# Performance work log

Measured on AMD Instinct MI355X. Metric: run time of the kernel, lower is better.

Reference implementation:

```python
import jax, jax.numpy as jnp
import numpy as np

OBS_DIM = 512
ATTN_DIM = 128


def setup_inputs() -> dict:
    key = jax.random.key(0)
    k1, k2, k3, k4 = jax.random.split(key, 4)
    agent_observation = jax.random.normal(k1, (128, 32, 512), dtype=jnp.float32)
    visible_observations = jax.random.normal(k2, (128, 32, 16, 512), dtype=jnp.float32)
    # learned bilinear projection params (match torch.randn init)
    w_psi = jax.random.normal(k3, (OBS_DIM, ATTN_DIM), dtype=jnp.float32)
    w_phi = jax.random.normal(k4, (OBS_DIM, ATTN_DIM), dtype=jnp.float32)
    return {
        "agent_observation": agent_observation,
        "visible_observations": visible_observations,
        "w_psi": w_psi,
        "w_phi": w_phi,
    }


def reference(agent_observation, visible_observations, w_psi, w_phi):
    # beta[b,e,a] = agent_obs[b,e] @ W_psi @ W_phi^T @ visible[b,e,a]
    q = jnp.einsum("bed,dk->bek", agent_observation, w_psi)          # (B,E,K)
    kv = jnp.einsum("bead,dk->beak", visible_observations, w_phi)    # (B,E,A,K)
    betas = jnp.einsum("bek,beak->bea", q, kv)                       # (B,E,A)
    # softmax over the visible-agent axis (the inner loop axis, dim=1 of
    # the per-entity stacked beta matrix in the original code)
    return jax.nn.softmax(betas, axis=-1)
```

## Files before the change

### kernel.cpp

```cpp
#include <hip/hip_runtime.h>
#include <math.h>

#define OBS 512
#define ATT 128
#define RPB 4

__global__ void transpose_wphi_k(const float* __restrict__ wphi,
                                 float* __restrict__ wphiT) {
  int idx = blockIdx.x * 256 + threadIdx.x;
  int k  = idx >> 9;
  int dd = idx & 511;
  wphiT[idx] = wphi[dd * ATT + k];
}

__device__ __forceinline__ void fma4(float4& a, float s, float4 w) {
  a.x = fmaf(s, w.x, a.x);
  a.y = fmaf(s, w.y, a.y);
  a.z = fmaf(s, w.z, a.z);
  a.w = fmaf(s, w.w, a.w);
}

__launch_bounds__(256, 4)
__global__ void entity_attn_k(const float* __restrict__ A,
                              const float* __restrict__ V,
                              const float* __restrict__ Wpsi,
                              const float* __restrict__ WphiT,
                              float* __restrict__ Out)
{
  __shared__ __align__(16) float S[6656];

  const int tid  = threadIdx.x;
  const int lane = tid & 63;
  const int wave = tid >> 6;
  const int g0   = blockIdx.x * RPB;

  {
    const int r = tid & 3;
    const int c = tid >> 2;
    const float4* a4 = (const float4*)(A + (size_t)(g0 + r) * OBS) + c * 2;
    float4 v0 = a4[0], v1 = a4[1];
    const int d0 = c * 8;
    S[(d0+0)*4+r] = v0.x; S[(d0+1)*4+r] = v0.y;
    S[(d0+2)*4+r] = v0.z; S[(d0+3)*4+r] = v0.w;
    S[(d0+4)*4+r] = v1.x; S[(d0+5)*4+r] = v1.y;
    S[(d0+6)*4+r] = v1.z; S[(d0+7)*4+r] = v1.w;
  }
  __syncthreads();

  {
    const int kg = tid & 31;
    const int ds = tid >> 5;
    float4 acc0 = make_float4(0.f,0.f,0.f,0.f);
    float4 acc1 = acc0, acc2 = acc0, acc3 = acc0;
    const float4* wp4 = (const float4*)Wpsi;
    const float4* at4 = (const float4*)S;
    const int dbase = ds * 64;
#pragma unroll 8
    for (int i = 0; i < 64; ++i) {
      const int d = dbase + i;
      float4 w = wp4[d * 32 + kg];
      float4 a = at4[d];
      fma4(acc0, a.x, w);
      fma4(acc1, a.y, w);
      fma4(acc2, a.z, w);
      fma4(acc3, a.w, w);
    }
    float4* qp4 = (float4*)(S + 2048);
    qp4[(ds*4+0)*32 + kg] = acc0;
    qp4[(ds*4+1)*32 + kg] = acc1;
    qp4[(ds*4+2)*32 + kg] = acc2;
    qp4[(ds*4+3)*32 + kg] = acc3;
  }
  __syncthreads();

  {
#pragma unroll
    for (int e = tid; e < 512; e += 256) {
      const int r = e & 3;
      const int k = e >> 2;
      float s = 0.f;
#pragma unroll
      for (int ds = 0; ds < 8; ++ds) s += S[2048 + (ds*4 + r)*128 + k];
      S[6144 + k*4 + r] = s;
    }
  }
  __syncthreads();

  {
    float acc[8] = {0.f,0.f,0.f,0.f,0.f,0.f,0.f,0.f};
    const float4* qt4 = (const float4*)(S + 6144);
#pragma unroll 4
    for (int k = 0; k < 128; ++k) {
      float w0 = WphiT[k*512 + tid];
      float w1 = WphiT[k*512 + tid + 256];
      float4 q = qt4[k];
      acc[0] = fmaf(q.x, w0, acc[0]);
      acc[1] = fmaf(q.y, w0, acc[1]);
      acc[2] = fmaf(q.z, w0, acc[2]);
      acc[3] = fmaf(q.w, w0, acc[3]);
      acc[4] = fmaf(q.x, w1, acc[4]);
      acc[5] = fmaf(q.y, w1, acc[5]);
      acc[6] = fmaf(q.z, w1, acc[6]);
      acc[7] = fmaf(q.w, w1, acc[7]);
    }
#pragma unroll
    for (int r = 0; r < 4; ++r) {
      S[r*512 + tid]       = acc[r];
      S[r*512 + tid + 256] = acc[4+r];
    }
  }
  __syncthreads();

  {
    const int r = wave;
    const size_t g = (size_t)(g0 + r);
    const float4* vrow = (const float4*)V + g * 2048;
    const float4* ur   = (const float4*)S + r * 128;
    const float4 uf0 = ur[lane*2];
    const float4 uf1 = ur[lane*2 + 1];
    float acc[16];
#pragma unroll
    for (int ag = 0; ag < 4; ++ag) {
      float4 va[8];
#pragma unroll
      for (int j = 0; j < 4; ++j) {
        va[j*2]   = vrow[(ag*4 + j)*128 + lane*2];
        va[j*2+1] = vrow[(ag*4 + j)*128 + lane*2 + 1];
      }
#pragma unroll
      for (int j = 0; j < 4; ++j) {
        float s;
        s = uf0.x * va[j*2].x;
        s = fmaf(uf0.y, va[j*2].y, s);
        s = fmaf(uf0.z, va[j*2].z, s);
        s = fmaf(uf0.w, va[j*2].w, s);
        s = fmaf(uf1.x, va[j*2+1].x, s);
        s = fmaf(uf1.y, va[j*2+1].y, s);
        s = fmaf(uf1.z, va[j*2+1].z, s);
        s = fmaf(uf1.w, va[j*2+1].w, s);
        acc[ag*4 + j] = s;
      }
    }
#pragma unroll
    for (int a = 0; a < 16; ++a) {
      float v = acc[a];
      v += __shfl_xor(v, 32, 64);
      v += __shfl_xor(v, 16, 64);
      v += __shfl_xor(v,  8, 64);
      v += __shfl_xor(v,  4, 64);
      v += __shfl_xor(v,  2, 64);
      v += __shfl_xor(v,  1, 64);
      acc[a] = v;
    }
    float mx = acc[0];
#pragma unroll
    for (int a = 1; a < 16; ++a) mx = fmaxf(mx, acc[a]);
    float ssum = 0.f;
#pragma unroll
    for (int a = 0; a < 16; ++a) { acc[a] = __expf(acc[a] - mx); ssum += acc[a]; }
    const float inv = 1.0f / ssum;
    if (lane == 0) {
      float4* o4 = (float4*)(Out + g * 16);
      o4[0] = make_float4(acc[0]*inv,  acc[1]*inv,  acc[2]*inv,  acc[3]*inv);
      o4[1] = make_float4(acc[4]*inv,  acc[5]*inv,  acc[6]*inv,  acc[7]*inv);
      o4[2] = make_float4(acc[8]*inv,  acc[9]*inv,  acc[10]*inv, acc[11]*inv);
      o4[3] = make_float4(acc[12]*inv, acc[13]*inv, acc[14]*inv, acc[15]*inv);
    }
  }
}

extern "C" void kernel_launch(void* const* d_in, const int* in_sizes, int n_in,
                              void* d_out, int out_size, void* d_ws, size_t ws_size,
                              hipStream_t stream) {
  (void)in_sizes; (void)n_in; (void)out_size; (void)ws_size;
  const float* A    = (const float*)d_in[0];
  const float* V    = (const float*)d_in[1];
  const float* Wpsi = (const float*)d_in[2];
  const float* Wphi = (const float*)d_in[3];
  float* Out   = (float*)d_out;
  float* WphiT = (float*)d_ws;

  transpose_wphi_k<<<256, 256, 0, stream>>>(Wphi, WphiT);
  entity_attn_k<<<1024, 256, 0, stream>>>(A, V, Wpsi, WphiT, Out);
}
```

Before: 52.11 us.

## Split fused kernel into projection kernel and streaming softmax kernel

Splits the single fused kernel into two. proj_k computes u = a·Wpsi·WphiT^T for 8 rows per block and writes it to workspace. stream_k then streams V, dots it with u and applies the softmax, issuing 8 rows of V loads per batch instead of 4. The aim is to take the compute-heavy projection off the bandwidth-bound streaming of V so the V loads are not stalled behind the projection phase and its barriers. In exchange it adds a kernel launch and a global round trip for U (2 MB written and read back).

```diff
diff --git a/kernel.cpp b/kernel.cpp
--- a/kernel.cpp
+++ b/kernel.cpp
@@ -3,7 +3,13 @@
 
 #define OBS 512
 #define ATT 128
-#define RPB 4
+
+__device__ __forceinline__ void fma4(float4& a, float s, const float4& w) {
+  a.x = fmaf(s, w.x, a.x);
+  a.y = fmaf(s, w.y, a.y);
+  a.z = fmaf(s, w.z, a.z);
+  a.w = fmaf(s, w.w, a.w);
+}
 
 __global__ void transpose_wphi_k(const float* __restrict__ wphi,
                                  float* __restrict__ wphiT) {
@@ -13,159 +19,145 @@
   wphiT[idx] = wphi[dd * ATT + k];
 }
 
-__device__ __forceinline__ void fma4(float4& a, float s, float4 w) {
-  a.x = fmaf(s, w.x, a.x);
-  a.y = fmaf(s, w.y, a.y);
-  a.z = fmaf(s, w.z, a.z);
-  a.w = fmaf(s, w.w, a.w);
-}
-
-__launch_bounds__(256, 4)
-__global__ void entity_attn_k(const float* __restrict__ A,
-                              const float* __restrict__ V,
-                              const float* __restrict__ Wpsi,
-                              const float* __restrict__ WphiT,
-                              float* __restrict__ Out)
+__launch_bounds__(256, 2)
+__global__ void proj_k(const float* __restrict__ A,
+                       const float* __restrict__ Wpsi,
+                       const float* __restrict__ WphiT,
+                       float* __restrict__ U)
 {
-  __shared__ __align__(16) float S[6656];
-
-  const int tid  = threadIdx.x;
-  const int lane = tid & 63;
-  const int wave = tid >> 6;
-  const int g0   = blockIdx.x * RPB;
+  __shared__ __align__(16) float As[8 * 512];
+  __shared__ __align__(16) float Qs[8 * 128];
+  const int tid = threadIdx.x;
+  const int g0  = blockIdx.x * 8;
 
   {
-    const int r = tid & 3;
-    const int c = tid >> 2;
-    const float4* a4 = (const float4*)(A + (size_t)(g0 + r) * OBS) + c * 2;
-    float4 v0 = a4[0], v1 = a4[1];
-    const int d0 = c * 8;
-    S[(d0+0)*4+r] = v0.x; S[(d0+1)*4+r] = v0.y;
-    S[(d0+2)*4+r] = v0.z; S[(d0+3)*4+r] = v0.w;
-    S[(d0+4)*4+r] = v1.x; S[(d0+5)*4+r] = v1.y;
-    S[(d0+6)*4+r] = v1.z; S[(d0+7)*4+r] = v1.w;
+    const float4* src = (const float4*)(A + (size_t)g0 * OBS);
+    float4* dst = (float4*)As;
+#pragma unroll
+    for (int j = 0; j < 4; ++j) dst[tid + j * 256] = src[tid + j * 256];
   }
   __syncthreads();
 
   {
     const int kg = tid & 31;
-    const int ds = tid >> 5;
-    float4 acc0 = make_float4(0.f,0.f,0.f,0.f);
-    float4 acc1 = acc0, acc2 = acc0, acc3 = acc0;
+    const int rg = tid >> 5;
+    float4 acc = make_float4(0.f, 0.f, 0.f, 0.f);
     const float4* wp4 = (const float4*)Wpsi;
-    const float4* at4 = (const float4*)S;
-    const int dbase = ds * 64;
-#pragma unroll 8
-    for (int i = 0; i < 64; ++i) {
-      const int d = dbase + i;
-      float4 w = wp4[d * 32 + kg];
-      float4 a = at4[d];
-      fma4(acc0, a.x, w);
-      fma4(acc1, a.y, w);
-      fma4(acc2, a.z, w);
-      fma4(acc3, a.w, w);
+    const float4* as4 = (const float4*)(As + rg * OBS);
+#pragma unroll 4
+    for (int dq = 0; dq < 128; ++dq) {
+      float4 av = as4[dq];
+      float4 w0 = wp4[(dq * 4 + 0) * 32 + kg];
+      float4 w1 = wp4[(dq * 4 + 1) * 32 + kg];
+      float4 w2 = wp4[(dq * 4 + 2) * 32 + kg];
+      float4 w3 = wp4[(dq * 4 + 3) * 32 + kg];
+      fma4(acc, av.x, w0);
+      fma4(acc, av.y, w1);
+      fma4(acc, av.z, w2);
+      fma4(acc, av.w, w3);
     }
-    float4* qp4 = (float4*)(S + 2048);
-    qp4[(ds*4+0)*32 + kg] = acc0;
-    qp4[(ds*4+1)*32 + kg] = acc1;
-    qp4[(ds*4+2)*32 + kg] = acc2;
-    qp4[(ds*4+3)*32 + kg] = acc3;
+    ((float4*)Qs)[rg * 32 + kg] = acc;
   }
   __syncthreads();
 
   {
+    const int cg = tid & 127;
+    const int rh = tid >> 7;
+    float4 acc[4];
 #pragma unroll
-    for (int e = tid; e < 512; e += 256) {
-      const int r = e & 3;
-      const int k = e >> 2;
-      float s = 0.f;
+    for (int i = 0; i < 4; ++i) acc[i] = make_float4(0.f, 0.f, 0.f, 0.f);
+    const float4* wt4 = (const float4*)WphiT;
+    const float4* qs4 = (const float4*)Qs;
+#pragma unroll 2
+    for (int kq = 0; kq < 32; ++kq) {
+      float4 q0 = qs4[(rh * 4 + 0) * 32 + kq];
+      float4 q1 = qs4[(rh * 4 + 1) * 32 + kq];
+      float4 q2 = qs4[(rh * 4 + 2) * 32 + kq];
+      float4 q3 = qs4[(rh * 4 + 3) * 32 + kq];
+      float qa[4] = {q0.x, q0.y, q0.z, q0.w};
+      float qb[4] = {q1.x, q1.y, q1.z, q1.w};
+      float qc[4] = {q2.x, q2.y, q2.z, q2.w};
+      float qd[4] = {q3.x, q3.y, q3.z, q3.w};
 #pragma unroll
-      for (int ds = 0; ds < 8; ++ds) s += S[2048 + (ds*4 + r)*128 + k];
-      S[6144 + k*4 + r] = s;
+      for (int j = 0; j < 4; ++j) {
+        float4 wt = wt4[(size_t)(kq * 4 + j) * 128 + cg];
+        fma4(acc[0], qa[j], wt);
+        fma4(acc[1], qb[j], wt);
+        fma4(acc[2], qc[j], wt);
+        fma4(acc[3], qd[j], wt);
+      }
+    }
+    float4* U4 = (float4*)U;
+#pragma unroll
+    for (int i = 0; i < 4; ++i)
+      U4[(size_t)(g0 + rh * 4 + i) * 128 + cg] = acc[i];
+  }
+}
+
+__launch_bounds__(256)
+__global__ void stream_k(const float* __restrict__ V,
+                         const float* __restrict__ U,
+                         float* __restrict__ Out)
+{
+  const int lane = threadIdx.x & 63;
+  const int wave = threadIdx.x >> 6;
+  const size_t g = (size_t)blockIdx.x * 4 + wave;
+
+  const float4* vrow = (const float4*)V + g * 2048;
+  const float4* ur   = (const float4*)U + g * 128;
+  const float4 uf0 = ur[lane * 2];
+  const float4 uf1 = ur[lane * 2 + 1];
+
+  float acc[16];
+#pragma unroll
+  for (int ag = 0; ag < 2; ++ag) {
+    float4 va[16];
+#pragma unroll
+    for (int j = 0; j < 8; ++j) {
+      va[j * 2]     = vrow[(size_t)(ag * 8 + j) * 128 + lane * 2];
+      va[j * 2 + 1] = vrow[(size_t)(ag * 8 + j) * 128 + lane * 2 + 1];
+    }
+#pragma unroll
+    for (int j = 0; j < 8; ++j) {
+      float s;
+      s = uf0.x * va[j * 2].x;
+      s = fmaf(uf0.y, va[j * 2].y, s);
+      s = fmaf(uf0.z, va[j * 2].z, s);
+      s = fmaf(uf0.w, va[j * 2].w, s);
+      s = fmaf(uf1.x, va[j * 2 + 1].x, s);
+      s = fmaf(uf1.y, va[j * 2 + 1].y, s);
+      s = fmaf(uf1.z, va[j * 2 + 1].z, s);
+      s = fmaf(uf1.w, va[j * 2 + 1].w, s);
+      acc[ag * 8 + j] = s;
     }
   }
-  __syncthreads();
 
-  {
-    float acc[8] = {0.f,0.f,0.f,0.f,0.f,0.f,0.f,0.f};
-    const float4* qt4 = (const float4*)(S + 6144);
-#pragma unroll 4
-    for (int k = 0; k < 128; ++k) {
-      float w0 = WphiT[k*512 + tid];
-      float w1 = WphiT[k*512 + tid + 256];
-      float4 q = qt4[k];
-      acc[0] = fmaf(q.x, w0, acc[0]);
-      acc[1] = fmaf(q.y, w0, acc[1]);
-      acc[2] = fmaf(q.z, w0, acc[2]);
-      acc[3] = fmaf(q.w, w0, acc[3]);
-      acc[4] = fmaf(q.x, w1, acc[4]);
-      acc[5] = fmaf(q.y, w1, acc[5]);
-      acc[6] = fmaf(q.z, w1, acc[6]);
-      acc[7] = fmaf(q.w, w1, acc[7]);
-    }
 #pragma unroll
-    for (int r = 0; r < 4; ++r) {
-      S[r*512 + tid]       = acc[r];
-      S[r*512 + tid + 256] = acc[4+r];
-    }
+  for (int a = 0; a < 16; ++a) {
+    float v = acc[a];
+    v += __shfl_xor(v, 32, 64);
+    v += __shfl_xor(v, 16, 64);
+    v += __shfl_xor(v,  8, 64);
+    v += __shfl_xor(v,  4, 64);
+    v += __shfl_xor(v,  2, 64);
+    v += __shfl_xor(v,  1, 64);
+    acc[a] = v;
   }
-  __syncthreads();
 
-  {
-    const int r = wave;
-    const size_t g = (size_t)(g0 + r);
-    const float4* vrow = (const float4*)V + g * 2048;
-    const float4* ur   = (const float4*)S + r * 128;
-    const float4 uf0 = ur[lane*2];
-    const float4 uf1 = ur[lane*2 + 1];
-    float acc[16];
+  float mx = acc[0];
 #pragma unroll
-    for (int ag = 0; ag < 4; ++ag) {
-      float4 va[8];
+  for (int a = 1; a < 16; ++a) mx = fmaxf(mx, acc[a]);
+  float ssum = 0.f;
 #pragma unroll
-      for (int j = 0; j < 4; ++j) {
-        va[j*2]   = vrow[(ag*4 + j)*128 + lane*2];
-        va[j*2+1] = vrow[(ag*4 + j)*128 + lane*2 + 1];
-      }
-#pragma unroll
-      for (int j = 0; j < 4; ++j) {
-        float s;
-        s = uf0.x * va[j*2].x;
-        s = fmaf(uf0.y, va[j*2].y, s);
-        s = fmaf(uf0.z, va[j*2].z, s);
-        s = fmaf(uf0.w, va[j*2].w, s);
-        s = fmaf(uf1.x, va[j*2+1].x, s);
-        s = fmaf(uf1.y, va[j*2+1].y, s);
-        s = fmaf(uf1.z, va[j*2+1].z, s);
-        s = fmaf(uf1.w, va[j*2+1].w, s);
-        acc[ag*4 + j] = s;
-      }
-    }
-#pragma unroll
-    for (int a = 0; a < 16; ++a) {
-      float v = acc[a];
-      v += __shfl_xor(v, 32, 64);
-      v += __shfl_xor(v, 16, 64);
-      v += __shfl_xor(v,  8, 64);
-      v += __shfl_xor(v,  4, 64);
-      v += __shfl_xor(v,  2, 64);
-      v += __shfl_xor(v,  1, 64);
-      acc[a] = v;
-    }
-    float mx = acc[0];
-#pragma unroll
-    for (int a = 1; a < 16; ++a) mx = fmaxf(mx, acc[a]);
-    float ssum = 0.f;
-#pragma unroll
-    for (int a = 0; a < 16; ++a) { acc[a] = __expf(acc[a] - mx); ssum += acc[a]; }
-    const float inv = 1.0f / ssum;
-    if (lane == 0) {
-      float4* o4 = (float4*)(Out + g * 16);
-      o4[0] = make_float4(acc[0]*inv,  acc[1]*inv,  acc[2]*inv,  acc[3]*inv);
-      o4[1] = make_float4(acc[4]*inv,  acc[5]*inv,  acc[6]*inv,  acc[7]*inv);
-      o4[2] = make_float4(acc[8]*inv,  acc[9]*inv,  acc[10]*inv, acc[11]*inv);
-      o4[3] = make_float4(acc[12]*inv, acc[13]*inv, acc[14]*inv, acc[15]*inv);
-    }
+  for (int a = 0; a < 16; ++a) { acc[a] = __expf(acc[a] - mx); ssum += acc[a]; }
+  const float inv = 1.0f / ssum;
+
+  if (lane == 0) {
+    float4* o4 = (float4*)(Out + g * 16);
+    o4[0] = make_float4(acc[0]*inv,  acc[1]*inv,  acc[2]*inv,  acc[3]*inv);
+    o4[1] = make_float4(acc[4]*inv,  acc[5]*inv,  acc[6]*inv,  acc[7]*inv);
+    o4[2] = make_float4(acc[8]*inv,  acc[9]*inv,  acc[10]*inv, acc[11]*inv);
+    o4[3] = make_float4(acc[12]*inv, acc[13]*inv, acc[14]*inv, acc[15]*inv);
   }
 }
 
@@ -178,8 +170,11 @@
   const float* Wpsi = (const float*)d_in[2];
   const float* Wphi = (const float*)d_in[3];
   float* Out   = (float*)d_out;
+
   float* WphiT = (float*)d_ws;
+  float* U     = (float*)d_ws + 65536;
 
   transpose_wphi_k<<<256, 256, 0, stream>>>(Wphi, WphiT);
-  entity_attn_k<<<1024, 256, 0, stream>>>(A, V, Wpsi, WphiT, Out);
+  proj_k<<<512, 256, 0, stream>>>(A, Wpsi, WphiT, U);
+  stream_k<<<1024, 256, 0, stream>>>(V, U, Out);
 }
```

Result: slower. 84.30 us (+61.8%).
